# Performance work log

Measured on AMD Instinct MI355X. Metric: run time of the kernel, lower is better.

The kernel has to match this reference:

```python
import jax, jax.numpy as jnp
import numpy as np

B, N, NY = 2, 4096, 4096
ENC_DIM, DEC_DIM, H = 768, 512, 8
HEAD_DIM = DEC_DIM // H
SCALE = HEAD_DIM ** -0.5


def setup_inputs() -> dict:
    key = jax.random.key(0)
    ks = jax.random.split(key, 8)
    lim_q = 1.0 / np.sqrt(DEC_DIM)
    lim_kv = 1.0 / np.sqrt(ENC_DIM)
    return {
        "x": jax.random.normal(ks[0], (B, N, DEC_DIM), jnp.float32),
        "y": jax.random.normal(ks[1], (B, NY, ENC_DIM), jnp.float32),
        "key_padding_mask": jax.random.randint(ks[2], (B, NY), 0, 2).astype(bool),
        "Wq": jax.random.uniform(ks[3], (DEC_DIM, DEC_DIM), jnp.float32, -lim_q, lim_q),
        "Wkv": jax.random.uniform(ks[4], (2 * DEC_DIM, ENC_DIM), jnp.float32, -lim_kv, lim_kv),
        "Wp": jax.random.uniform(ks[5], (DEC_DIM, DEC_DIM), jnp.float32, -lim_q, lim_q),
        "bp": jax.random.uniform(ks[6], (DEC_DIM,), jnp.float32, -lim_q, lim_q),
    }


def reference(x, y, key_padding_mask, Wq, Wkv, Wp, bp):
    # q projection: [B,N,C] -> [B,H,N,D]
    q = (x @ Wq.T).reshape(B, N, H, HEAD_DIM).transpose(0, 2, 1, 3)
    # kv projection: [B,Ny,E] -> [B,Ny,2C] -> k,v each [B,H,Ny,D]
    kv = (y @ Wkv.T).reshape(B, NY, 2, H, HEAD_DIM).transpose(2, 0, 3, 1, 4)
    k, v = kv[0], kv[1]
    # attention scores [B,H,N,Ny]
    attn = jnp.einsum("bhnd,bhmd->bhnm", q, k) * SCALE
    attn = jnp.where(key_padding_mask[:, None, None, :], -jnp.inf, attn)
    attn = jax.nn.softmax(attn, axis=-1)
    out = jnp.einsum("bhnm,bhmd->bhnd", attn, v)  # [B,H,N,D]
    out = out.transpose(0, 2, 1, 3).reshape(B, N, DEC_DIM)
    return out @ Wp.T + bp
```

## Files before the change

kernel.cpp:

```cpp
#include <hip/hip_runtime.h>
#include <hip/hip_bf16.h>
#include <stdint.h>

typedef __bf16 bf16_t;
typedef __bf16 bf16x8 __attribute__((ext_vector_type(8)));
typedef __bf16 bf16x4 __attribute__((ext_vector_type(4)));
typedef float  f32x4  __attribute__((ext_vector_type(4)));

#define MFMA16(a, b, c) __builtin_amdgcn_mfma_f32_16x16x32_bf16((a), (b), (c), 0, 0, 0)

__device__ __forceinline__ void gload_lds16(const void* g, void* l) {
  __builtin_amdgcn_global_load_lds((const __attribute__((address_space(1))) void*)g,
                                   (__attribute__((address_space(3))) void*)l, 16, 0, 0);
}

#define QSCALE 0.18033688011112042f
#define NE_X   4194304UL
#define NE_Y   6291456UL
#define NE_WQ  262144UL
#define NE_WKV 786432UL
#define NE_WP  262144UL
#define NE_BP  512UL

__global__ void detect_and_mask(const uint16_t* __restrict__ xu,
                                const uint8_t* __restrict__ mk,
                                int* __restrict__ flags, bf16_t* __restrict__ mmul) {
  __shared__ int cbf, c3f1, c3f3, cnz;
  const int t = threadIdx.x;
  if (t == 0) { cbf = 0; c3f1 = 0; c3f3 = 0; cnz = 0; }
  __syncthreads();
  if (blockIdx.x == 0) {
    int local = 0;
    for (int i = t; i < 2048; i += 256) {
      uint16_t u = xu[2 * i];
      int e = (u >> 7) & 0xFF;
      if (u == 0 || (e >= 0x66 && e <= 0x88)) local++;
    }
    atomicAdd(&cbf, local);
  }
  int l1 = 0, l3 = 0, lnz = 0;
  for (int i = t; i < 4096; i += 256) {
    uint8_t b = mk[i];
    int p = i & 3;
    if (p == 1 && b == 0x3F) l1++;
    if (p == 3 && b == 0x3F) l3++;
    if (p != 0 && b != 0) lnz++;
  }
  atomicAdd(&c3f1, l1);
  atomicAdd(&c3f3, l3);
  atomicAdd(&cnz, lnz);
  __syncthreads();
  if (blockIdx.x == 0 && t == 0) flags[0] = (cbf > 1536) ? 1 : 0;
  const int fmt = (c3f1 > 0) ? 2 : (c3f3 > 0) ? 3 : (cnz > 0) ? 0 : 1;
  const int i = blockIdx.x * 256 + t;
  bool on;
  if (fmt == 0)      on = mk[i] != 0;
  else if (fmt == 1) on = ((const int*)mk)[i] != 0;
  else if (fmt == 2) on = (((const uint16_t*)mk)[i] & 0x7FFF) != 0;
  else               on = ((const float*)mk)[i] != 0.0f;
  mmul[i] = on ? (bf16_t)0.0f : (bf16_t)1.0f;
}

__global__ void convert_all(const void* __restrict__ x, const void* __restrict__ y,
                            const void* __restrict__ wq, const void* __restrict__ wkv,
                            const void* __restrict__ wp, const void* __restrict__ bp,
                            uint16_t* __restrict__ dst, const int* __restrict__ flags) {
  const size_t E0 = NE_X, E1 = E0 + NE_Y, E2 = E1 + NE_WQ, E3 = E2 + NE_WKV,
               E4 = E3 + NE_WP, E5 = E4 + NE_BP;
  size_t i8 = ((size_t)blockIdx.x * 256 + threadIdx.x) * 8;
  if (i8 >= E5) return;
  const void* src; size_t off;
  if      (i8 < E0) { src = x;   off = i8; }
  else if (i8 < E1) { src = y;   off = i8 - E0; }
  else if (i8 < E2) { src = wq;  off = i8 - E1; }
  else if (i8 < E3) { src = wkv; off = i8 - E2; }
  else if (i8 < E4) { src = wp;  off = i8 - E3; }
  else              { src = bp;  off = i8 - E4; }
  const bool isWq = (i8 >= E1 && i8 < E2);
  if (flags[0] && !isWq) {
    *(uint4*)(dst + i8) = *(const uint4*)((const uint16_t*)src + off);
    return;
  }
  float v[8];
  if (flags[0]) {
    const uint16_t* u = (const uint16_t*)src + off;
    for (int j = 0; j < 8; ++j) {
      union { uint32_t q; float f; } c; c.q = ((uint32_t)u[j]) << 16; v[j] = c.f;
    }
  } else {
    const float* f = (const float*)src + off;
    float4 a = *(const float4*)f;
    float4 b2 = *(const float4*)(f + 4);
    v[0] = a.x; v[1] = a.y; v[2] = a.z; v[3] = a.w;
    v[4] = b2.x; v[5] = b2.y; v[6] = b2.z; v[7] = b2.w;
  }
  const float sc = isWq ? QSCALE : 1.0f;
  union { bf16_t h[8]; uint4 u; } pk;
  for (int j = 0; j < 8; ++j) pk.h[j] = (bf16_t)(v[j] * sc);
  *(uint4*)(dst + i8) = pk.u;
}

template <int K, int MODE>
__launch_bounds__(256, 2)
__global__ void gemm_bt(const bf16_t* __restrict__ A, const bf16_t* __restrict__ W,
                        const bf16_t* __restrict__ bias, void* __restrict__ C,
                        bf16_t* __restrict__ Vt, const int* __restrict__ flags, int Ncols) {
  __shared__ __align__(16) char lds[16384];
  char* ldsA = lds;
  char* ldsW = lds + 8192;
  const int t = threadIdx.x;
  const int w = t >> 6, lane = t & 63, quad = lane >> 4, l16 = lane & 15;
  const int wr = w >> 1, wc = w & 1;
  const int m0 = blockIdx.y * 128, n0 = blockIdx.x * 128;

  f32x4 acc[4][4] = {};
  const int rowS = t >> 2, uS = t & 3;

  for (int k0 = 0; k0 < K; k0 += 32) {
    __syncthreads();
    for (int i = 0; i < 2; ++i) {
      int row = i * 64 + rowS;
      int c = uS ^ ((row >> 1) & 3);
      gload_lds16(A + (size_t)(m0 + row) * K + k0 + c * 8, ldsA + i * 4096 + w * 1024);
      gload_lds16(W + (size_t)(n0 + row) * K + k0 + c * 8, ldsW + i * 4096 + w * 1024);
    }
    __syncthreads();
    bf16x8 af[4], bfr[4];
    for (int mt = 0; mt < 4; ++mt) {
      int row = wr * 64 + mt * 16 + l16;
      int us = quad ^ ((row >> 1) & 3);
      af[mt] = *(const bf16x8*)(ldsA + row * 64 + us * 16);
    }
    for (int nt = 0; nt < 4; ++nt) {
      int row = wc * 64 + nt * 16 + l16;
      int us = quad ^ ((row >> 1) & 3);
      bfr[nt] = *(const bf16x8*)(ldsW + row * 64 + us * 16);
    }
    for (int mt = 0; mt < 4; ++mt)
      for (int nt = 0; nt < 4; ++nt)
        acc[mt][nt] = MFMA16(af[mt], bfr[nt], acc[mt][nt]);
  }

  const int mbase = m0 + wr * 64;
  for (int nt = 0; nt < 4; ++nt) {
    const int col = n0 + wc * 64 + nt * 16 + l16;
    if (MODE == 1 && col >= 512) {
      const int hd = col - 512;
      const int hh = hd >> 6, d = hd & 63;
      const int dt = d >> 4, l15 = d & 15;
      for (int mt = 0; mt < 4; ++mt) {
        int m = mbase + mt * 16 + quad * 4;
        int bb = m >> 12, keyg = m & 4095;
        int kt = keyg >> 6, keyin = keyg & 63;
        int kc = (keyin >> 5) & 1, jq = (keyin >> 3) & 3, j0 = keyin & 7;
        const bf16_t* mmp = bias + bb * 4096 + keyg;
        union { bf16_t h4[4]; uint2 u; } pk;
        for (int r = 0; r < 4; ++r) pk.h4[r] = (bf16_t)(acc[mt][nt][r] * (float)mmp[r]);
        size_t base = (((size_t)(bb * 8 + hh) * 64 + kt) * 8 + dt * 2 + kc) * 1024
                      + (jq * 16 + l15) * 16 + j0 * 2;
        *(uint2*)((char*)Vt + base) = pk.u;
      }
    } else if (MODE == 1) {
      for (int mt = 0; mt < 4; ++mt) {
        int m = mbase + mt * 16 + quad * 4;
        for (int r = 0; r < 4; ++r)
          ((bf16_t*)C)[(size_t)(m + r) * 512 + col] = (bf16_t)acc[mt][nt][r];
      }
    } else if (MODE == 0) {
      for (int mt = 0; mt < 4; ++mt) {
        int m = mbase + mt * 16 + quad * 4;
        for (int r = 0; r < 4; ++r)
          ((bf16_t*)C)[(size_t)(m + r) * Ncols + col] = (bf16_t)acc[mt][nt][r];
      }
    } else {
      const float bv = (float)bias[col];
      const bool obf = (flags[0] != 0);
      for (int mt = 0; mt < 4; ++mt) {
        int m = mbase + mt * 16 + quad * 4;
        for (int r = 0; r < 4; ++r) {
          float v = acc[mt][nt][r] + bv;
          if (obf) ((bf16_t*)C)[(size_t)(m + r) * Ncols + col] = (bf16_t)v;
          else     ((float*)C)[(size_t)(m + r) * Ncols + col] = v;
        }
      }
    }
  }
}

__launch_bounds__(256, 2)
__global__ void attn(const bf16_t* __restrict__ Qb, const bf16_t* __restrict__ Kb,
                     const bf16_t* __restrict__ Vfb, const bf16_t* __restrict__ mmul,
                     bf16_t* __restrict__ Ob) {
  const int t = threadIdx.x, w = t >> 6, lane = t & 63, quad = lane >> 4, l16 = lane & 15;
  const int bid = blockIdx.x;
  const int h = bid & 7;
  const int b = (bid >> 3) & 1;
  const int q0 = (bid >> 4) * 128;

  __shared__ __align__(16) char lds[49152];
  char* Pw = lds + 32768 + w * 4096;
  char* Qs = lds + 32768;

  for (int i = 0; i < 4; ++i) {
    int row = i * 32 + (t >> 3);
    int c = (t & 7) ^ (row & 7);
    gload_lds16(Qb + (size_t)(b * 4096 + q0 + row) * 512 + h * 64 + c * 8,
                Qs + i * 4096 + w * 1024);
  }
  for (int kt = 0; kt < 2; ++kt)
    for (int i = 0; i < 2; ++i) {
      int row = i * 32 + (t >> 3);
      int c = (t & 7) ^ (row & 7);
      gload_lds16(Kb + (size_t)(b * 4096 + kt * 64 + row) * 512 + h * 64 + c * 8,
                  lds + kt * 8192 + i * 4096 + w * 1024);
    }
  __syncthreads();

  bf16x8 qf[2][2];
  for (int ng = 0; ng < 2; ++ng)
    for (int kc = 0; kc < 2; ++kc) {
      int row = 32 * w + 16 * ng + l16;
      int u = (4 * kc + quad) ^ (row & 7);
      qf[ng][kc] = *(const bf16x8*)(Qs + row * 128 + u * 16);
    }
  __syncthreads();

  f32x4 o[2][4] = {};
  f32x4 lacc[2] = {};
  const char* Vfbase = (const char*)Vfb + (size_t)(b * 8 + h) * 524288;

  for (int ktp = 0; ktp < 32; ++ktp) {
    const int ktA = ktp * 2;
    if (ktp + 1 < 32) {
      for (int kk = 2; kk < 4; ++kk) {
        const int kt = ktA + kk;
        for (int i = 0; i < 2; ++i) {
          int row = i * 32 + (t >> 3);
          int c = (t & 7) ^ (row & 7);
          gload_lds16(Kb + (size_t)(b * 4096 + kt * 64 + row) * 512 + h * 64 + c * 8,
                      lds + (kt & 3) * 8192 + i * 4096 + w * 1024);
        }
      }
    }
#pragma unroll
    for (int kk = 0; kk < 2; ++kk) {
      const int kt = ktA + kk;
      const int kt0 = kt * 64;
      const char* Kl = lds + (kt & 3) * 8192;

      bf16x8 mf[2];
      mf[0] = *(const bf16x8*)(mmul + b * 4096 + kt0 + quad * 8);
      mf[1] = *(const bf16x8*)(mmul + b * 4096 + kt0 + 32 + quad * 8);
      const char* Vtile = Vfbase + (size_t)kt * 8192;
      bf16x8 vf[4][2];
      for (int dt = 0; dt < 4; ++dt)
        for (int kc = 0; kc < 2; ++kc)
          vf[dt][kc] = *(const bf16x8*)(Vtile + (dt * 2 + kc) * 1024 + lane * 16);

      bf16x8 kf[4][2];
      for (int mt = 0; mt < 4; ++mt)
        for (int kc = 0; kc < 2; ++kc) {
          int row = mt * 16 + l16;
          int u = (4 * kc + quad) ^ (row & 7);
          kf[mt][kc] = *(const bf16x8*)(Kl + row * 128 + u * 16);
        }

      f32x4 z[2][4];
      __builtin_amdgcn_s_setprio(1);
      for (int ng = 0; ng < 2; ++ng)
        for (int mt = 0; mt < 4; ++mt) {
          f32x4 zz = {};
          zz = MFMA16(kf[mt][0], qf[ng][0], zz);
          z[ng][mt] = MFMA16(kf[mt][1], qf[ng][1], zz);
        }
      __builtin_amdgcn_s_setprio(0);

      for (int ng = 0; ng < 2; ++ng) {
        const int row = 16 * ng + l16;
        for (int mt = 0; mt < 4; ++mt) {
          bf16x4 pk;
          pk.x = (bf16_t)__builtin_amdgcn_exp2f(z[ng][mt][0]);
          pk.y = (bf16_t)__builtin_amdgcn_exp2f(z[ng][mt][1]);
          pk.z = (bf16_t)__builtin_amdgcn_exp2f(z[ng][mt][2]);
          pk.w = (bf16_t)__builtin_amdgcn_exp2f(z[ng][mt][3]);
          int c2 = (2 * mt + (quad >> 1)) ^ (row & 7);
          *(bf16x4*)(Pw + row * 128 + c2 * 16 + (quad & 1) * 8) = pk;
        }
      }

      bf16x8 pf[2][2];
      for (int ng = 0; ng < 2; ++ng)
        for (int kc = 0; kc < 2; ++kc) {
          int row = 16 * ng + l16;
          int u = (4 * kc + quad) ^ (row & 7);
          pf[ng][kc] = *(const bf16x8*)(Pw + row * 128 + u * 16);
        }
      __builtin_amdgcn_s_setprio(1);
      for (int ng = 0; ng < 2; ++ng) {
        lacc[ng] = MFMA16(pf[ng][0], mf[0], lacc[ng]);
        lacc[ng] = MFMA16(pf[ng][1], mf[1], lacc[ng]);
      }
      for (int dt = 0; dt < 4; ++dt)
        for (int kc = 0; kc < 2; ++kc) {
          o[0][dt] = MFMA16(pf[0][kc], vf[dt][kc], o[0][dt]);
          o[1][dt] = MFMA16(pf[1][kc], vf[dt][kc], o[1][dt]);
        }
      __builtin_amdgcn_s_setprio(0);
    }
    __syncthreads();
  }

  for (int ng = 0; ng < 2; ++ng) {
    float inv[4];
    for (int r = 0; r < 4; ++r) inv[r] = 1.0f / lacc[ng][r];
    for (int dt = 0; dt < 4; ++dt)
      for (int r = 0; r < 4; ++r) {
        int q = q0 + 32 * w + 16 * ng + quad * 4 + r;
        int col = h * 64 + dt * 16 + l16;
        Ob[(size_t)(b * 4096 + q) * 512 + col] = (bf16_t)(o[ng][dt][r] * inv[r]);
      }
  }
}

extern "C" void kernel_launch(void* const* d_in, const int* in_sizes, int n_in,
                              void* d_out, int out_size, void* d_ws, size_t ws_size,
                              hipStream_t stream) {
  const void* x   = d_in[0];
  const void* y   = d_in[1];
  const void* msk = d_in[2];
  const void* Wq  = d_in[3];
  const void* Wkv = d_in[4];
  const void* Wp  = d_in[5];
  const void* bp  = d_in[6];

  char* ws = (char*)d_ws;
  bf16_t* Xb   = (bf16_t*)(ws + 0);
  bf16_t* Yb   = (bf16_t*)(ws + 8388608);
  bf16_t* Wqb  = (bf16_t*)(ws + 20971520);
  bf16_t* Wkvb = (bf16_t*)(ws + 21495808);
  bf16_t* Wpb  = (bf16_t*)(ws + 23068672);
  bf16_t* bpb  = (bf16_t*)(ws + 23592960);
  bf16_t* mmul = (bf16_t*)(ws + 23593984);
  int*    flags = (int*)(ws + 23610368);
  bf16_t* Kbuf  = (bf16_t*)(ws + 25165824);
  bf16_t* Vfrag = (bf16_t*)(ws + 33554432);
  bf16_t* Qbuf  = (bf16_t*)(ws + 8388608);
  bf16_t* Obuf  = (bf16_t*)(ws + 0);

  hipLaunchKernelGGL(detect_and_mask, dim3(32), dim3(256), 0, stream,
                     (const uint16_t*)x, (const uint8_t*)msk, flags, mmul);
  hipLaunchKernelGGL(convert_all, dim3(5761), dim3(256), 0, stream,
                     x, y, Wq, Wkv, Wp, bp, (uint16_t*)ws, flags);
  hipLaunchKernelGGL((gemm_bt<768, 1>), dim3(8, 64), dim3(256), 0, stream,
                     Yb, Wkvb, mmul, (void*)Kbuf, Vfrag, flags, 1024);
  hipLaunchKernelGGL((gemm_bt<512, 0>), dim3(4, 64), dim3(256), 0, stream,
                     Xb, Wqb, (const bf16_t*)nullptr, (void*)Qbuf, (bf16_t*)nullptr, flags, 512);
  hipLaunchKernelGGL(attn, dim3(512), dim3(256), 0, stream,
                     Qbuf, Kbuf, Vfrag, mmul, Obuf);
  hipLaunchKernelGGL((gemm_bt<512, 2>), dim3(4, 64), dim3(256), 0, stream,
                     Obuf, Wpb, bpb, d_out, (bf16_t*)nullptr, flags, 512);
}
```

Baseline: 238.2 us.

## Transpose P in registers with permlane swaps and deepen K prefetch ring

The softmax probability tile is now converted from the QK^T MFMA output layout into the A-operand layout with v_permlane32/16_swap instead of a round trip through per-wave LDS, which removes LDS writes and reads on the critical path. The K ring buffer grows from 4 to 8 tiles, processing 4 tiles per iteration with 4 prefetched ahead, so there are half as many block barriers. LDS use rises to 64KB, which may limit occupancy at 2 blocks per CU. The permlane lane mapping has to match the MFMA operand layout exactly for the results to stay correct.

```diff
diff --git a/kernel.cpp b/kernel.cpp
--- a/kernel.cpp
+++ b/kernel.cpp
@@ -12,6 +12,20 @@
 __device__ __forceinline__ void gload_lds16(const void* g, void* l) {
   __builtin_amdgcn_global_load_lds((const __attribute__((address_space(1))) void*)g,
                                    (__attribute__((address_space(3))) void*)l, 16, 0, 0);
+}
+
+__device__ __forceinline__ void permlane32_swap(uint32_t& a, uint32_t& b) {
+  asm("v_permlane32_swap_b32 %0, %1" : "+v"(a), "+v"(b));
+}
+__device__ __forceinline__ void permlane16_swap(uint32_t& a, uint32_t& b) {
+  asm("v_permlane16_swap_b32 %0, %1" : "+v"(a), "+v"(b));
+}
+
+__device__ __forceinline__ uint32_t pack_e2(float a, float b) {
+  union { bf16_t h[2]; uint32_t u; } p;
+  p.h[0] = (bf16_t)__builtin_amdgcn_exp2f(a);
+  p.h[1] = (bf16_t)__builtin_amdgcn_exp2f(b);
+  return p.u;
 }
 
 #define QSCALE 0.18033688011112042f
@@ -197,8 +211,7 @@
   const int b = (bid >> 3) & 1;
   const int q0 = (bid >> 4) * 128;
 
-  __shared__ __align__(16) char lds[49152];
-  char* Pw = lds + 32768 + w * 4096;
+  __shared__ __align__(16) char lds[65536];
   char* Qs = lds + 32768;
 
   for (int i = 0; i < 4; ++i) {
@@ -207,7 +220,7 @@
     gload_lds16(Qb + (size_t)(b * 4096 + q0 + row) * 512 + h * 64 + c * 8,
                 Qs + i * 4096 + w * 1024);
   }
-  for (int kt = 0; kt < 2; ++kt)
+  for (int kt = 0; kt < 4; ++kt)
     for (int i = 0; i < 2; ++i) {
       int row = i * 32 + (t >> 3);
       int c = (t & 7) ^ (row & 7);
@@ -229,24 +242,24 @@
   f32x4 lacc[2] = {};
   const char* Vfbase = (const char*)Vfb + (size_t)(b * 8 + h) * 524288;
 
-  for (int ktp = 0; ktp < 32; ++ktp) {
-    const int ktA = ktp * 2;
-    if (ktp + 1 < 32) {
-      for (int kk = 2; kk < 4; ++kk) {
+  for (int ktg = 0; ktg < 16; ++ktg) {
+    const int ktA = ktg * 4;
+    if (ktg + 1 < 16) {
+      for (int kk = 4; kk < 8; ++kk) {
         const int kt = ktA + kk;
         for (int i = 0; i < 2; ++i) {
           int row = i * 32 + (t >> 3);
           int c = (t & 7) ^ (row & 7);
           gload_lds16(Kb + (size_t)(b * 4096 + kt * 64 + row) * 512 + h * 64 + c * 8,
-                      lds + (kt & 3) * 8192 + i * 4096 + w * 1024);
+                      lds + (kt & 7) * 8192 + i * 4096 + w * 1024);
         }
       }
     }
 #pragma unroll
-    for (int kk = 0; kk < 2; ++kk) {
+    for (int kk = 0; kk < 4; ++kk) {
       const int kt = ktA + kk;
       const int kt0 = kt * 64;
-      const char* Kl = lds + (kt & 3) * 8192;
+      const char* Kl = lds + (kt & 7) * 8192;
 
       bf16x8 mf[2];
       mf[0] = *(const bf16x8*)(mmul + b * 4096 + kt0 + quad * 8);
@@ -265,36 +278,32 @@
           kf[mt][kc] = *(const bf16x8*)(Kl + row * 128 + u * 16);
         }
 
-      f32x4 z[2][4];
-      __builtin_amdgcn_s_setprio(1);
-      for (int ng = 0; ng < 2; ++ng)
+      bf16x8 pf[2][2];
+      for (int ng = 0; ng < 2; ++ng) {
+        f32x4 z[4];
+        __builtin_amdgcn_s_setprio(1);
         for (int mt = 0; mt < 4; ++mt) {
           f32x4 zz = {};
           zz = MFMA16(kf[mt][0], qf[ng][0], zz);
-          z[ng][mt] = MFMA16(kf[mt][1], qf[ng][1], zz);
-        }
-      __builtin_amdgcn_s_setprio(0);
-
-      for (int ng = 0; ng < 2; ++ng) {
-        const int row = 16 * ng + l16;
+          z[mt] = MFMA16(kf[mt][1], qf[ng][1], zz);
+        }
+        __builtin_amdgcn_s_setprio(0);
+        uint32_t w0[4], w1[4];
         for (int mt = 0; mt < 4; ++mt) {
-          bf16x4 pk;
-          pk.x = (bf16_t)__builtin_amdgcn_exp2f(z[ng][mt][0]);
-          pk.y = (bf16_t)__builtin_amdgcn_exp2f(z[ng][mt][1]);
-          pk.z = (bf16_t)__builtin_amdgcn_exp2f(z[ng][mt][2]);
-          pk.w = (bf16_t)__builtin_amdgcn_exp2f(z[ng][mt][3]);
-          int c2 = (2 * mt + (quad >> 1)) ^ (row & 7);
-          *(bf16x4*)(Pw + row * 128 + c2 * 16 + (quad & 1) * 8) = pk;
-        }
-      }
-
-      bf16x8 pf[2][2];
-      for (int ng = 0; ng < 2; ++ng)
+          w0[mt] = pack_e2(z[mt][0], z[mt][1]);
+          w1[mt] = pack_e2(z[mt][2], z[mt][3]);
+        }
         for (int kc = 0; kc < 2; ++kc) {
-          int row = 16 * ng + l16;
-          int u = (4 * kc + quad) ^ (row & 7);
-          pf[ng][kc] = *(const bf16x8*)(Pw + row * 128 + u * 16);
-        }
+          uint32_t a0 = w0[2 * kc], b0 = w0[2 * kc + 1];
+          uint32_t a1 = w1[2 * kc], b1 = w1[2 * kc + 1];
+          permlane32_swap(a0, b0); permlane16_swap(a0, b0);
+          permlane32_swap(a1, b1); permlane16_swap(a1, b1);
+          union { uint32_t u[4]; bf16x8 v; } P;
+          P.u[0] = a0; P.u[1] = a1; P.u[2] = b0; P.u[3] = b1;
+          pf[ng][kc] = P.v;
+        }
+      }
+
       __builtin_amdgcn_s_setprio(1);
       for (int ng = 0; ng < 2; ++ng) {
         lacc[ng] = MFMA16(pf[ng][0], mf[0], lacc[ng]);
```

Result: slower. 245.3 us (+3.0%).

## Stage V tiles in LDS and split attention over eight waves

Applied to the files above, without the earlier changes.

The attention kernel now uses 512-thread blocks with eight waves, each owning 16 query rows instead of 32. V fragments are staged asynchronously into a 4-slot LDS ring alongside K, rather than each wave reading them from global memory. This cuts redundant global/L2 traffic for V and adds latency-hiding waves per block. In exchange, LDS per block grows to 80KB and K fragments read from LDS are reused across fewer query rows per wave.

```diff
diff --git a/kernel.cpp b/kernel.cpp
--- a/kernel.cpp
+++ b/kernel.cpp
@@ -187,7 +187,7 @@
   }
 }
 
-__launch_bounds__(256, 2)
+__launch_bounds__(512, 4)
 __global__ void attn(const bf16_t* __restrict__ Qb, const bf16_t* __restrict__ Kb,
                      const bf16_t* __restrict__ Vfb, const bf16_t* __restrict__ mmul,
                      bf16_t* __restrict__ Ob) {
@@ -197,127 +197,111 @@
   const int b = (bid >> 3) & 1;
   const int q0 = (bid >> 4) * 128;
 
-  __shared__ __align__(16) char lds[49152];
-  char* Pw = lds + 32768 + w * 4096;
-  char* Qs = lds + 32768;
-
-  for (int i = 0; i < 4; ++i) {
-    int row = i * 32 + (t >> 3);
-    int c = (t & 7) ^ (row & 7);
+  __shared__ __align__(16) char lds[81920];
+  char* Pw = lds + 65536 + w * 2048;
+  char* Qs = lds + 65536;
+
+  const bf16_t* Kbase = Kb + (size_t)(b * 4096) * 512 + h * 64;
+  const char* Vfbase = (const char*)Vfb + (size_t)(b * 8 + h) * 524288;
+
+  const int srow = w * 8 + (lane >> 3);
+  const int sc8 = (lane & 7);
+
+  auto stage_tile = [&](int kt) {
+    char* slot = lds + (kt & 3) * 16384;
+    int c = sc8 ^ (srow & 7);
+    gload_lds16(Kbase + (size_t)(kt * 64 + srow) * 512 + c * 8, slot + w * 1024);
+    gload_lds16(Vfbase + (size_t)kt * 8192 + w * 1024 + lane * 16,
+                slot + 8192 + w * 1024);
+  };
+
+  for (int i = 0; i < 2; ++i) {
+    int row = i * 64 + srow;
+    int c = sc8 ^ (row & 7);
     gload_lds16(Qb + (size_t)(b * 4096 + q0 + row) * 512 + h * 64 + c * 8,
-                Qs + i * 4096 + w * 1024);
-  }
-  for (int kt = 0; kt < 2; ++kt)
-    for (int i = 0; i < 2; ++i) {
-      int row = i * 32 + (t >> 3);
-      int c = (t & 7) ^ (row & 7);
-      gload_lds16(Kb + (size_t)(b * 4096 + kt * 64 + row) * 512 + h * 64 + c * 8,
-                  lds + kt * 8192 + i * 4096 + w * 1024);
-    }
+                Qs + i * 8192 + w * 1024);
+  }
+  stage_tile(0);
+  stage_tile(1);
   __syncthreads();
 
-  bf16x8 qf[2][2];
-  for (int ng = 0; ng < 2; ++ng)
-    for (int kc = 0; kc < 2; ++kc) {
-      int row = 32 * w + 16 * ng + l16;
-      int u = (4 * kc + quad) ^ (row & 7);
-      qf[ng][kc] = *(const bf16x8*)(Qs + row * 128 + u * 16);
-    }
+  const int u0 = quad ^ (l16 & 7), u1 = (4 + quad) ^ (l16 & 7);
+  bf16x8 qf[2];
+  {
+    int row = w * 16 + l16;
+    qf[0] = *(const bf16x8*)(Qs + row * 128 + u0 * 16);
+    qf[1] = *(const bf16x8*)(Qs + row * 128 + u1 * 16);
+  }
   __syncthreads();
 
-  f32x4 o[2][4] = {};
-  f32x4 lacc[2] = {};
-  const char* Vfbase = (const char*)Vfb + (size_t)(b * 8 + h) * 524288;
-
-  for (int ktp = 0; ktp < 32; ++ktp) {
-    const int ktA = ktp * 2;
-    if (ktp + 1 < 32) {
-      for (int kk = 2; kk < 4; ++kk) {
-        const int kt = ktA + kk;
-        for (int i = 0; i < 2; ++i) {
-          int row = i * 32 + (t >> 3);
-          int c = (t & 7) ^ (row & 7);
-          gload_lds16(Kb + (size_t)(b * 4096 + kt * 64 + row) * 512 + h * 64 + c * 8,
-                      lds + (kt & 3) * 8192 + i * 4096 + w * 1024);
-        }
-      }
-    }
-#pragma unroll
-    for (int kk = 0; kk < 2; ++kk) {
-      const int kt = ktA + kk;
-      const int kt0 = kt * 64;
-      const char* Kl = lds + (kt & 3) * 8192;
-
-      bf16x8 mf[2];
-      mf[0] = *(const bf16x8*)(mmul + b * 4096 + kt0 + quad * 8);
-      mf[1] = *(const bf16x8*)(mmul + b * 4096 + kt0 + 32 + quad * 8);
-      const char* Vtile = Vfbase + (size_t)kt * 8192;
-      bf16x8 vf[4][2];
-      for (int dt = 0; dt < 4; ++dt)
-        for (int kc = 0; kc < 2; ++kc)
-          vf[dt][kc] = *(const bf16x8*)(Vtile + (dt * 2 + kc) * 1024 + lane * 16);
-
-      bf16x8 kf[4][2];
-      for (int mt = 0; mt < 4; ++mt)
-        for (int kc = 0; kc < 2; ++kc) {
-          int row = mt * 16 + l16;
-          int u = (4 * kc + quad) ^ (row & 7);
-          kf[mt][kc] = *(const bf16x8*)(Kl + row * 128 + u * 16);
-        }
-
-      f32x4 z[2][4];
-      __builtin_amdgcn_s_setprio(1);
-      for (int ng = 0; ng < 2; ++ng)
-        for (int mt = 0; mt < 4; ++mt) {
-          f32x4 zz = {};
-          zz = MFMA16(kf[mt][0], qf[ng][0], zz);
-          z[ng][mt] = MFMA16(kf[mt][1], qf[ng][1], zz);
-        }
-      __builtin_amdgcn_s_setprio(0);
-
-      for (int ng = 0; ng < 2; ++ng) {
-        const int row = 16 * ng + l16;
-        for (int mt = 0; mt < 4; ++mt) {
-          bf16x4 pk;
-          pk.x = (bf16_t)__builtin_amdgcn_exp2f(z[ng][mt][0]);
-          pk.y = (bf16_t)__builtin_amdgcn_exp2f(z[ng][mt][1]);
-          pk.z = (bf16_t)__builtin_amdgcn_exp2f(z[ng][mt][2]);
-          pk.w = (bf16_t)__builtin_amdgcn_exp2f(z[ng][mt][3]);
-          int c2 = (2 * mt + (quad >> 1)) ^ (row & 7);
-          *(bf16x4*)(Pw + row * 128 + c2 * 16 + (quad & 1) * 8) = pk;
-        }
-      }
-
-      bf16x8 pf[2][2];
-      for (int ng = 0; ng < 2; ++ng)
-        for (int kc = 0; kc < 2; ++kc) {
-          int row = 16 * ng + l16;
-          int u = (4 * kc + quad) ^ (row & 7);
-          pf[ng][kc] = *(const bf16x8*)(Pw + row * 128 + u * 16);
-        }
-      __builtin_amdgcn_s_setprio(1);
-      for (int ng = 0; ng < 2; ++ng) {
-        lacc[ng] = MFMA16(pf[ng][0], mf[0], lacc[ng]);
-        lacc[ng] = MFMA16(pf[ng][1], mf[1], lacc[ng]);
-      }
-      for (int dt = 0; dt < 4; ++dt)
-        for (int kc = 0; kc < 2; ++kc) {
-          o[0][dt] = MFMA16(pf[0][kc], vf[dt][kc], o[0][dt]);
-          o[1][dt] = MFMA16(pf[1][kc], vf[dt][kc], o[1][dt]);
-        }
-      __builtin_amdgcn_s_setprio(0);
-    }
+  f32x4 o[4] = {};
+  f32x4 lacc = {};
+
+  auto process = [&](int kt) {
+    const char* slot = lds + (kt & 3) * 16384;
+    const int kt0 = kt * 64;
+    bf16x8 mf0 = *(const bf16x8*)(mmul + b * 4096 + kt0 + quad * 8);
+    bf16x8 mf1 = *(const bf16x8*)(mmul + b * 4096 + kt0 + 32 + quad * 8);
+    bf16x8 kf[4][2];
+    for (int mt = 0; mt < 4; ++mt) {
+      kf[mt][0] = *(const bf16x8*)(slot + (mt * 16 + l16) * 128 + u0 * 16);
+      kf[mt][1] = *(const bf16x8*)(slot + (mt * 16 + l16) * 128 + u1 * 16);
+    }
+    f32x4 z[4];
+    __builtin_amdgcn_s_setprio(1);
+    for (int mt = 0; mt < 4; ++mt) {
+      f32x4 zz = {};
+      zz = MFMA16(kf[mt][0], qf[0], zz);
+      z[mt] = MFMA16(kf[mt][1], qf[1], zz);
+    }
+    __builtin_amdgcn_s_setprio(0);
+    for (int mt = 0; mt < 4; ++mt) {
+      bf16x4 pk;
+      pk.x = (bf16_t)__builtin_amdgcn_exp2f(z[mt][0]);
+      pk.y = (bf16_t)__builtin_amdgcn_exp2f(z[mt][1]);
+      pk.z = (bf16_t)__builtin_amdgcn_exp2f(z[mt][2]);
+      pk.w = (bf16_t)__builtin_amdgcn_exp2f(z[mt][3]);
+      int c2 = (2 * mt + (quad >> 1)) ^ (l16 & 7);
+      *(bf16x4*)(Pw + l16 * 128 + c2 * 16 + (quad & 1) * 8) = pk;
+    }
+    const char* Vs = slot + 8192;
+    bf16x8 vf[4][2];
+    for (int dt = 0; dt < 4; ++dt) {
+      vf[dt][0] = *(const bf16x8*)(Vs + (dt * 2 + 0) * 1024 + lane * 16);
+      vf[dt][1] = *(const bf16x8*)(Vs + (dt * 2 + 1) * 1024 + lane * 16);
+    }
+    bf16x8 pf[2];
+    pf[0] = *(const bf16x8*)(Pw + l16 * 128 + u0 * 16);
+    pf[1] = *(const bf16x8*)(Pw + l16 * 128 + u1 * 16);
+    __builtin_amdgcn_s_setprio(1);
+    lacc = MFMA16(pf[0], mf0, lacc);
+    lacc = MFMA16(pf[1], mf1, lacc);
+    for (int dt = 0; dt < 4; ++dt) {
+      o[dt] = MFMA16(pf[0], vf[dt][0], o[dt]);
+      o[dt] = MFMA16(pf[1], vf[dt][1], o[dt]);
+    }
+    __builtin_amdgcn_s_setprio(0);
+  };
+
+  for (int pg = 0; pg < 32; ++pg) {
+    const int ktA = pg * 2;
+    if (pg + 1 < 32) {
+      stage_tile(ktA + 2);
+      stage_tile(ktA + 3);
+    }
+    process(ktA);
+    process(ktA + 1);
     __syncthreads();
   }
 
-  for (int ng = 0; ng < 2; ++ng) {
+  {
     float inv[4];
-    for (int r = 0; r < 4; ++r) inv[r] = 1.0f / lacc[ng][r];
+    for (int r = 0; r < 4; ++r) inv[r] = 1.0f / lacc[r];
     for (int dt = 0; dt < 4; ++dt)
       for (int r = 0; r < 4; ++r) {
-        int q = q0 + 32 * w + 16 * ng + quad * 4 + r;
+        int q = q0 + w * 16 + quad * 4 + r;
         int col = h * 64 + dt * 16 + l16;
-        Ob[(size_t)(b * 4096 + q) * 512 + col] = (bf16_t)(o[ng][dt][r] * inv[r]);
+        Ob[(size_t)(b * 4096 + q) * 512 + col] = (bf16_t)(o[dt][r] * inv[r]);
       }
   }
 }
@@ -355,7 +339,7 @@
                      Yb, Wkvb, mmul, (void*)Kbuf, Vfrag, flags, 1024);
   hipLaunchKernelGGL((gemm_bt<512, 0>), dim3(4, 64), dim3(256), 0, stream,
                      Xb, Wqb, (const bf16_t*)nullptr, (void*)Qbuf, (bf16_t*)nullptr, flags, 512);
-  hipLaunchKernelGGL(attn, dim3(512), dim3(256), 0, stream,
+  hipLaunchKernelGGL(attn, dim3(512), dim3(512), 0, stream,
                      Qbuf, Kbuf, Vfrag, mmul, Obuf);
   hipLaunchKernelGGL((gemm_bt<512, 2>), dim3(4, 64), dim3(256), 0, stream,
                      Obuf, Wpb, bpb, d_out, (bf16_t*)nullptr, flags, 512);
```

New measurement: 241.6 us. Within noise of the previous version (+1.5%).

## Double attention block size and deepen K-tile LDS ring with vmcnt-based pipelining

Applied to the files above, without the earlier changes.

Each attention block now has 512 threads covering 256 queries, so each K tile loaded into LDS is shared by twice as many waves and the grid halves. K staging becomes a 10-slot LDS ring with 8 tiles in flight. The loop waits on vmcnt counts and raw s_barrier instead of __syncthreads. LDS use grows to 112 KB per block, which likely limits occupancy to one block per CU and adds risk around the hand-counted waitcnt synchronisation.

```diff
diff --git a/kernel.cpp b/kernel.cpp
--- a/kernel.cpp
+++ b/kernel.cpp
@@ -187,7 +187,7 @@
   }
 }
 
-__launch_bounds__(256, 2)
+__launch_bounds__(512, 2)
 __global__ void attn(const bf16_t* __restrict__ Qb, const bf16_t* __restrict__ Kb,
                      const bf16_t* __restrict__ Vfb, const bf16_t* __restrict__ mmul,
                      bf16_t* __restrict__ Ob) {
@@ -195,119 +195,118 @@
   const int bid = blockIdx.x;
   const int h = bid & 7;
   const int b = (bid >> 3) & 1;
-  const int q0 = (bid >> 4) * 128;
-
-  __shared__ __align__(16) char lds[49152];
-  char* Pw = lds + 32768 + w * 4096;
-  char* Qs = lds + 32768;
-
+  const int q0 = (bid >> 4) * 256;
+
+  __shared__ __align__(16) char lds[114688];
+  char* Pw = lds + 81920 + w * 4096;
+  char* Qs = lds + 49152;
+
+  const bf16_t* Kbase = Kb + (size_t)(b * 4096) * 512 + h * 64;
+  const char* Vfbase = (const char*)Vfb + (size_t)(b * 8 + h) * 524288;
+
+  const int srow = t >> 3;
+  const int sc8 = t & 7;
+
+  auto stage_tile = [&](int kt, int slot) {
+    int c = sc8 ^ (srow & 7);
+    gload_lds16(Kbase + (size_t)(kt * 64 + srow) * 512 + c * 8,
+                lds + slot * 8192 + w * 1024);
+  };
+
+  for (int kt = 0; kt < 6; ++kt) stage_tile(kt, kt);
   for (int i = 0; i < 4; ++i) {
-    int row = i * 32 + (t >> 3);
-    int c = (t & 7) ^ (row & 7);
+    int row = i * 64 + srow;
+    int c = sc8 ^ (row & 7);
     gload_lds16(Qb + (size_t)(b * 4096 + q0 + row) * 512 + h * 64 + c * 8,
-                Qs + i * 4096 + w * 1024);
-  }
-  for (int kt = 0; kt < 2; ++kt)
-    for (int i = 0; i < 2; ++i) {
-      int row = i * 32 + (t >> 3);
-      int c = (t & 7) ^ (row & 7);
-      gload_lds16(Kb + (size_t)(b * 4096 + kt * 64 + row) * 512 + h * 64 + c * 8,
-                  lds + kt * 8192 + i * 4096 + w * 1024);
-    }
-  __syncthreads();
+                Qs + i * 8192 + w * 1024);
+  }
+  asm volatile("s_waitcnt vmcnt(0)" ::: "memory");
+  __builtin_amdgcn_sched_barrier(0);
+  __builtin_amdgcn_s_barrier();
 
   bf16x8 qf[2][2];
   for (int ng = 0; ng < 2; ++ng)
     for (int kc = 0; kc < 2; ++kc) {
       int row = 32 * w + 16 * ng + l16;
-      int u = (4 * kc + quad) ^ (row & 7);
+      int u = (4 * kc + quad) ^ (l16 & 7);
       qf[ng][kc] = *(const bf16x8*)(Qs + row * 128 + u * 16);
     }
-  __syncthreads();
+  asm volatile("s_waitcnt lgkmcnt(0)" ::: "memory");
+  __builtin_amdgcn_sched_barrier(0);
+  __builtin_amdgcn_s_barrier();
+  stage_tile(6, 6);
+  stage_tile(7, 7);
 
   f32x4 o[2][4] = {};
   f32x4 lacc[2] = {};
-  const char* Vfbase = (const char*)Vfb + (size_t)(b * 8 + h) * 524288;
-
-  for (int ktp = 0; ktp < 32; ++ktp) {
-    const int ktA = ktp * 2;
-    if (ktp + 1 < 32) {
-      for (int kk = 2; kk < 4; ++kk) {
-        const int kt = ktA + kk;
-        for (int i = 0; i < 2; ++i) {
-          int row = i * 32 + (t >> 3);
-          int c = (t & 7) ^ (row & 7);
-          gload_lds16(Kb + (size_t)(b * 4096 + kt * 64 + row) * 512 + h * 64 + c * 8,
-                      lds + (kt & 3) * 8192 + i * 4096 + w * 1024);
-        }
-      }
-    }
-#pragma unroll
-    for (int kk = 0; kk < 2; ++kk) {
-      const int kt = ktA + kk;
-      const int kt0 = kt * 64;
-      const char* Kl = lds + (kt & 3) * 8192;
-
-      bf16x8 mf[2];
-      mf[0] = *(const bf16x8*)(mmul + b * 4096 + kt0 + quad * 8);
-      mf[1] = *(const bf16x8*)(mmul + b * 4096 + kt0 + 32 + quad * 8);
-      const char* Vtile = Vfbase + (size_t)kt * 8192;
-      bf16x8 vf[4][2];
-      for (int dt = 0; dt < 4; ++dt)
-        for (int kc = 0; kc < 2; ++kc)
-          vf[dt][kc] = *(const bf16x8*)(Vtile + (dt * 2 + kc) * 1024 + lane * 16);
-
-      bf16x8 kf[4][2];
-      for (int mt = 0; mt < 4; ++mt)
-        for (int kc = 0; kc < 2; ++kc) {
-          int row = mt * 16 + l16;
-          int u = (4 * kc + quad) ^ (row & 7);
-          kf[mt][kc] = *(const bf16x8*)(Kl + row * 128 + u * 16);
-        }
-
-      f32x4 z[2][4];
+  const int u0 = quad ^ (l16 & 7), u1 = (4 + quad) ^ (l16 & 7);
+
+  auto process = [&](int kt, int slot) {
+    const int kt0 = kt * 64;
+    bf16x8 mf0 = *(const bf16x8*)(mmul + b * 4096 + kt0 + quad * 8);
+    bf16x8 mf1 = *(const bf16x8*)(mmul + b * 4096 + kt0 + 32 + quad * 8);
+    const char* Vtile = Vfbase + (size_t)kt * 8192;
+    bf16x8 vf[4][2];
+    for (int dt = 0; dt < 4; ++dt)
+      for (int kc = 0; kc < 2; ++kc)
+        vf[dt][kc] = *(const bf16x8*)(Vtile + (dt * 2 + kc) * 1024 + lane * 16);
+    const char* Kl = lds + slot * 8192;
+    bf16x8 kf[4][2];
+    for (int mt = 0; mt < 4; ++mt) {
+      kf[mt][0] = *(const bf16x8*)(Kl + (mt * 16 + l16) * 128 + u0 * 16);
+      kf[mt][1] = *(const bf16x8*)(Kl + (mt * 16 + l16) * 128 + u1 * 16);
+    }
+    f32x4 z[2][4];
+    __builtin_amdgcn_s_setprio(1);
+    for (int ng = 0; ng < 2; ++ng)
+      for (int mt = 0; mt < 4; ++mt) {
+        f32x4 zz = {};
+        zz = MFMA16(kf[mt][0], qf[ng][0], zz);
+        z[ng][mt] = MFMA16(kf[mt][1], qf[ng][1], zz);
+      }
+    __builtin_amdgcn_s_setprio(0);
+    for (int ng = 0; ng < 2; ++ng) {
+      char* Pn = Pw + ng * 2048;
+      for (int mt = 0; mt < 4; ++mt) {
+        bf16x4 pk;
+        pk.x = (bf16_t)__builtin_amdgcn_exp2f(z[ng][mt][0]);
+        pk.y = (bf16_t)__builtin_amdgcn_exp2f(z[ng][mt][1]);
+        pk.z = (bf16_t)__builtin_amdgcn_exp2f(z[ng][mt][2]);
+        pk.w = (bf16_t)__builtin_amdgcn_exp2f(z[ng][mt][3]);
+        int c2 = (2 * mt + (quad >> 1)) ^ (l16 & 7);
+        *(bf16x4*)(Pn + l16 * 128 + c2 * 16 + (quad & 1) * 8) = pk;
+      }
+      bf16x8 pf0 = *(const bf16x8*)(Pn + l16 * 128 + u0 * 16);
+      bf16x8 pf1 = *(const bf16x8*)(Pn + l16 * 128 + u1 * 16);
       __builtin_amdgcn_s_setprio(1);
-      for (int ng = 0; ng < 2; ++ng)
-        for (int mt = 0; mt < 4; ++mt) {
-          f32x4 zz = {};
-          zz = MFMA16(kf[mt][0], qf[ng][0], zz);
-          z[ng][mt] = MFMA16(kf[mt][1], qf[ng][1], zz);
-        }
+      lacc[ng] = MFMA16(pf0, mf0, lacc[ng]);
+      lacc[ng] = MFMA16(pf1, mf1, lacc[ng]);
+      for (int dt = 0; dt < 4; ++dt) {
+        o[ng][dt] = MFMA16(pf0, vf[dt][0], o[ng][dt]);
+        o[ng][dt] = MFMA16(pf1, vf[dt][1], o[ng][dt]);
+      }
       __builtin_amdgcn_s_setprio(0);
-
-      for (int ng = 0; ng < 2; ++ng) {
-        const int row = 16 * ng + l16;
-        for (int mt = 0; mt < 4; ++mt) {
-          bf16x4 pk;
-          pk.x = (bf16_t)__builtin_amdgcn_exp2f(z[ng][mt][0]);
-          pk.y = (bf16_t)__builtin_amdgcn_exp2f(z[ng][mt][1]);
-          pk.z = (bf16_t)__builtin_amdgcn_exp2f(z[ng][mt][2]);
-          pk.w = (bf16_t)__builtin_amdgcn_exp2f(z[ng][mt][3]);
-          int c2 = (2 * mt + (quad >> 1)) ^ (row & 7);
-          *(bf16x4*)(Pw + row * 128 + c2 * 16 + (quad & 1) * 8) = pk;
-        }
-      }
-
-      bf16x8 pf[2][2];
-      for (int ng = 0; ng < 2; ++ng)
-        for (int kc = 0; kc < 2; ++kc) {
-          int row = 16 * ng + l16;
-          int u = (4 * kc + quad) ^ (row & 7);
-          pf[ng][kc] = *(const bf16x8*)(Pw + row * 128 + u * 16);
-        }
-      __builtin_amdgcn_s_setprio(1);
-      for (int ng = 0; ng < 2; ++ng) {
-        lacc[ng] = MFMA16(pf[ng][0], mf[0], lacc[ng]);
-        lacc[ng] = MFMA16(pf[ng][1], mf[1], lacc[ng]);
-      }
-      for (int dt = 0; dt < 4; ++dt)
-        for (int kc = 0; kc < 2; ++kc) {
-          o[0][dt] = MFMA16(pf[0][kc], vf[dt][kc], o[0][dt]);
-          o[1][dt] = MFMA16(pf[1][kc], vf[dt][kc], o[1][dt]);
-        }
-      __builtin_amdgcn_s_setprio(0);
-    }
-    __syncthreads();
+    }
+  };
+
+  int sA = 0, sB = 1;
+  for (int pg = 0; pg < 32; ++pg) {
+    if (pg < 29) { asm volatile("s_waitcnt vmcnt(6)" ::: "memory"); }
+    else         { asm volatile("s_waitcnt vmcnt(0)" ::: "memory"); }
+    __builtin_amdgcn_sched_barrier(0);
+    __builtin_amdgcn_s_barrier();
+    const int ktA = pg * 2;
+    process(ktA, sA);
+    process(ktA + 1, sB);
+    if (ktA + 8 < 64) {
+      int s8A = sA + 8; if (s8A >= 10) s8A -= 10;
+      int s8B = sB + 8; if (s8B >= 10) s8B -= 10;
+      stage_tile(ktA + 8, s8A);
+      stage_tile(ktA + 9, s8B);
+    }
+    __builtin_amdgcn_s_barrier();
+    sA += 2; if (sA >= 10) sA -= 10;
+    sB += 2; if (sB >= 10) sB -= 10;
   }
 
   for (int ng = 0; ng < 2; ++ng) {
@@ -355,7 +354,7 @@
                      Yb, Wkvb, mmul, (void*)Kbuf, Vfrag, flags, 1024);
   hipLaunchKernelGGL((gemm_bt<512, 0>), dim3(4, 64), dim3(256), 0, stream,
                      Xb, Wqb, (const bf16_t*)nullptr, (void*)Qbuf, (bf16_t*)nullptr, flags, 512);
-  hipLaunchKernelGGL(attn, dim3(512), dim3(256), 0, stream,
+  hipLaunchKernelGGL(attn, dim3(256), dim3(512), 0, stream,
                      Qbuf, Kbuf, Vfrag, mmul, Obuf);
   hipLaunchKernelGGL((gemm_bt<512, 2>), dim3(4, 64), dim3(256), 0, stream,
                      Obuf, Wpb, bpb, d_out, (bf16_t*)nullptr, flags, 512);
```

After: 238.9 us. Within noise of the previous version (+0.3%).
